# Optimization experiments

Measured on AMD Instinct MI355X. Metric: run time of the kernel, lower is better.

Reference implementation:

```python
import jax, jax.numpy as jnp
import numpy as np

N_NODES = 100000
N_EDGES = 300000
N_GRAPHS = 2048
IN_DIM = 38
HID = 256
LAYERS = 5
OUT_DIM = 1
BN_EPS = 1e-5


def setup_inputs() -> dict:
    key = jax.random.key(0)
    ks = jax.random.split(key, 20)
    x = jax.random.normal(ks[0], (N_NODES, IN_DIM), dtype=jnp.float32)
    edge_index = jax.random.randint(ks[1], (2, N_EDGES), 0, N_NODES, dtype=jnp.int32)
    batch = jnp.sort(jax.random.randint(ks[2], (N_NODES,), 0, N_GRAPHS, dtype=jnp.int32))
    s_in = 1.0 / np.sqrt(IN_DIM)
    s_h = 1.0 / np.sqrt(HID)
    return {
        "x": x,
        "edge_index": edge_index,
        "batch": batch,
        "Wp": jax.random.uniform(ks[3], (IN_DIM, HID), jnp.float32, -s_in, s_in),
        "bp": jnp.zeros((HID,), jnp.float32),
        "eps": jnp.zeros((LAYERS,), jnp.float32),  # train_eps=True, init 0
        "W1s": jax.random.uniform(ks[4], (LAYERS, HID, HID), jnp.float32, -s_h, s_h),
        "b1s": jnp.zeros((LAYERS, HID), jnp.float32),
        "W2s": jax.random.uniform(ks[5], (LAYERS, HID, HID), jnp.float32, -s_h, s_h),
        "b2s": jnp.zeros((LAYERS, HID), jnp.float32),
        "gammas": jnp.ones((LAYERS, HID), jnp.float32),
        "betas": jnp.zeros((LAYERS, HID), jnp.float32),
        "Wr1": jax.random.uniform(ks[6], (HID, HID), jnp.float32, -s_h, s_h),
        "br1": jnp.zeros((HID,), jnp.float32),
        "Wr2": jax.random.uniform(ks[7], (HID, OUT_DIM), jnp.float32, -s_h, s_h),
        "br2": jnp.zeros((OUT_DIM,), jnp.float32),
    }


def _forward(x, edge_index, batch, Wp, bp, eps, W1s, b1s, W2s, b2s,
             gammas, betas, Wr1, br1, Wr2, br2):
    src, dst = edge_index[0], edge_index[1]
    h = x @ Wp + bp  # [N, HID]
    for l in range(LAYERS):
        # GINConv: (1+eps)*h_i + sum_{j->i} h_j  (scatter-add over edges)
        agg = jnp.zeros_like(h).at[dst].add(h[src])
        z = (1.0 + eps[l]) * h + agg
        # 2-layer MLP
        z = jax.nn.relu(z @ W1s[l] + b1s[l]) @ W2s[l] + b2s[l]
        # BatchNorm1d (training-mode batch statistics, biased variance)
        mu = jnp.mean(z, axis=0)
        var = jnp.var(z, axis=0)
        z = (z - mu) * jax.lax.rsqrt(var + BN_EPS) * gammas[l] + betas[l]
        h = jax.nn.relu(z)  # dropout disabled (eval)
    # global mean pool over graphs
    sums = jax.ops.segment_sum(h, batch, num_segments=N_GRAPHS)
    counts = jax.ops.segment_sum(jnp.ones((h.shape[0],), h.dtype), batch,
                                 num_segments=N_GRAPHS)
    pooled = sums / jnp.maximum(counts, 1.0)[:, None]
    # readout MLP (dropout disabled)
    out = jax.nn.relu(pooled @ Wr1 + br1) @ Wr2 + br2
    return out  # [N_GRAPHS, OUT_DIM]


def reference(x, edge_index, batch, Wp, bp, eps, W1s, b1s, W2s, b2s,
              gammas, betas, Wr1, br1, Wr2, br2):
    return _forward(x, edge_index, batch, Wp, bp, eps, W1s, b1s, W2s, b2s,
                    gammas, betas, Wr1, br1, Wr2, br2)
```

## Files before the change

kernel.cpp:

```cpp
#include <hip/hip_runtime.h>

#define N_NODES 100000
#define N_EDGES 300000
#define N_GRAPHS 2048
#define IN_DIM 38
#define HID 256
#define LAYERS 5
#define BN_EPS 1e-5f

#define SCAN_CHUNK 512
#define N_CHUNKS ((N_NODES + SCAN_CHUNK - 1) / SCAN_CHUNK)

#define ROW_PAD 128

typedef unsigned short u16;
typedef unsigned int u32;
typedef __attribute__((ext_vector_type(8))) short short8;
typedef __attribute__((ext_vector_type(4))) unsigned short ushortx4;
typedef __attribute__((ext_vector_type(4))) unsigned int uintx4;
typedef __attribute__((ext_vector_type(4))) float floatx4;

__device__ __forceinline__ unsigned short bf16_rne(float f) {
    unsigned int u = __float_as_uint(f);
    unsigned int r = (u + 0x7fffu + ((u >> 16) & 1u)) >> 16;
    return (unsigned short)r;
}
__device__ __forceinline__ float uf(unsigned short b) {
    return __uint_as_float((unsigned int)b << 16);
}
__device__ __forceinline__ float unpack_pair(u32 w) {
    return uf((unsigned short)(w & 0xffffu)) + uf((unsigned short)(w >> 16));
}
__device__ __forceinline__ void split_bf16(float v, unsigned short& hi,
                                           unsigned short& lo) {
    hi = bf16_rne(v);
    float hf = __uint_as_float((unsigned int)hi << 16);
    lo = (unsigned short)(__float_as_uint(v - hf) >> 16);
}
__device__ __forceinline__ u32 pack_pair(float v) {
    unsigned short hb, lb;
    split_bf16(v, hb, lb);
    return (u32)hb | ((u32)lb << 16);
}
__device__ __forceinline__ void load16_to_lds(const void* g, void* l) {
    __builtin_amdgcn_global_load_lds(
        (const __attribute__((address_space(1))) unsigned int*)g,
        (__attribute__((address_space(3))) unsigned int*)l, 16, 0, 0);
}
__device__ __forceinline__ void bn_params(const float* sums, const float* sumsq,
                                          const float* gammas,
                                          const float* betas, int c, float& sc,
                                          float& sh) {
    const float invN = 1.0f / (float)N_NODES;
    float mu = sums[c] * invN;
    float var = sumsq[c] * invN - mu * mu;
    float rs = rsqrtf(var + BN_EPS);
    float g = gammas[c];
    sc = rs * g;
    sh = betas[c] - mu * rs * g;
}

#define PROJ_CH 64
__global__ __launch_bounds__(256) void proj_kernel(
    const float* __restrict__ x, const float* __restrict__ Wp,
    const float* __restrict__ bp, u32* __restrict__ h) {
    __shared__ float xs[PROJ_CH * IN_DIM];
    int t = threadIdx.x;
    float w[IN_DIM];
#pragma unroll
    for (int k = 0; k < IN_DIM; k++) w[k] = Wp[k * HID + t];
    float b = bp[t];
    int n0 = blockIdx.x * PROJ_CH;
    int count = min(PROJ_CH, N_NODES - n0);
    int total = count * IN_DIM;
    const float* xbase = x + (size_t)n0 * IN_DIM;
    for (int i = t; i < total; i += 256) xs[i] = xbase[i];
    __syncthreads();
    for (int n = 0; n < count; n++) {
        float acc = b;
        const float* xr = &xs[n * IN_DIM];
#pragma unroll
        for (int k = 0; k < IN_DIM; k++) acc = fmaf(xr[k], w[k], acc);
        h[(size_t)(n0 + n) * 256 + t] = pack_pair(acc);
    }
}

__global__ __launch_bounds__(256) void hist_kernel(const int* __restrict__ ei,
                                                   int* __restrict__ deg) {
    int e = blockIdx.x * 256 + threadIdx.x;
    if (e < N_EDGES) atomicAdd(&deg[ei[N_EDGES + e]], 1);
}

__global__ __launch_bounds__(256) void scan1_kernel(const int* __restrict__ deg,
                                                    int* __restrict__ offs,
                                                    int* __restrict__ blocksums) {
    __shared__ int s[SCAN_CHUNK];
    int base = blockIdx.x * SCAN_CHUNK;
    int t = threadIdx.x;
    int i0 = t, i1 = t + 256;
    int g0 = base + i0, g1 = base + i1;
    int o0 = (g0 < N_NODES) ? deg[g0] : 0;
    int o1 = (g1 < N_NODES) ? deg[g1] : 0;
    s[i0] = o0;
    s[i1] = o1;
    __syncthreads();
    for (int off = 1; off < SCAN_CHUNK; off <<= 1) {
        int v0 = (i0 >= off) ? s[i0 - off] : 0;
        int v1 = (i1 >= off) ? s[i1 - off] : 0;
        __syncthreads();
        s[i0] += v0;
        s[i1] += v1;
        __syncthreads();
    }
    if (g0 < N_NODES) offs[g0] = s[i0] - o0;
    if (g1 < N_NODES) offs[g1] = s[i1] - o1;
    if (t == 0) blocksums[blockIdx.x] = s[SCAN_CHUNK - 1];
}

__global__ __launch_bounds__(256) void scan2_kernel(int* __restrict__ blocksums) {
    __shared__ int s[256];
    int t = threadIdx.x;
    int o = (t < N_CHUNKS) ? blocksums[t] : 0;
    s[t] = o;
    __syncthreads();
    for (int off = 1; off < 256; off <<= 1) {
        int v = (t >= off) ? s[t - off] : 0;
        __syncthreads();
        s[t] += v;
        __syncthreads();
    }
    if (t < N_CHUNKS) blocksums[t] = s[t] - o;
}

__global__ __launch_bounds__(256) void scan3_kernel(int* __restrict__ offs,
                                                    const int* __restrict__ blocksums,
                                                    int* __restrict__ cursor) {
    int g = blockIdx.x * 256 + threadIdx.x;
    if (g < N_NODES) {
        int v = offs[g] + blocksums[g / SCAN_CHUNK];
        offs[g] = v;
        cursor[g] = v;
    }
    if (g == 0) offs[N_NODES] = N_EDGES;
}

__global__ __launch_bounds__(256) void fill_kernel(const int* __restrict__ ei,
                                                   int* __restrict__ cursor,
                                                   int* __restrict__ csr_src) {
    int e = blockIdx.x * 256 + threadIdx.x;
    if (e < N_EDGES) {
        int src = ei[e];
        int dst = ei[N_EDGES + e];
        int pos = atomicAdd(&cursor[dst], 1);
        csr_src[pos] = src;
    }
}

__global__ __launch_bounds__(256) void gather_kernel(
    const int* __restrict__ offs, const int* __restrict__ csr_src,
    const u32* __restrict__ zin, u16* __restrict__ zout,
    const float* __restrict__ eps, int layer,
    const float* __restrict__ sums, const float* __restrict__ sumsq,
    const float* __restrict__ gammas, const float* __restrict__ betas,
    int useBN) {
    int wave = threadIdx.x >> 6;
    int lane = threadIdx.x & 63;
    int node = blockIdx.x * 4 + wave;
    if (node >= N_NODES) return;
    float s = 1.0f + eps[layer];
    int c0 = lane * 4;
    int beg = offs[node], end = offs[node + 1];
    uintx4 vself = *(const uintx4*)&zin[(size_t)node * 256 + c0];
    float4 sc = make_float4(1.f, 1.f, 1.f, 1.f);
    float4 sh = make_float4(0.f, 0.f, 0.f, 0.f);
    if (useBN) {
        bn_params(sums, sumsq, gammas, betas, c0 + 0, sc.x, sh.x);
        bn_params(sums, sumsq, gammas, betas, c0 + 1, sc.y, sh.y);
        bn_params(sums, sumsq, gammas, betas, c0 + 2, sc.z, sh.z);
        bn_params(sums, sumsq, gammas, betas, c0 + 3, sc.w, sh.w);
    }
    float acc[4];
    acc[0] = unpack_pair(vself[0]);
    acc[1] = unpack_pair(vself[1]);
    acc[2] = unpack_pair(vself[2]);
    acc[3] = unpack_pair(vself[3]);
    if (useBN) {
        acc[0] = fmaxf(acc[0] * sc.x + sh.x, 0.f);
        acc[1] = fmaxf(acc[1] * sc.y + sh.y, 0.f);
        acc[2] = fmaxf(acc[2] * sc.z + sh.z, 0.f);
        acc[3] = fmaxf(acc[3] * sc.w + sh.w, 0.f);
    }
    acc[0] *= s; acc[1] *= s; acc[2] *= s; acc[3] *= s;

    for (int base = beg; base < end; base += 4) {
        int i0 = csr_src[base];
        int i1 = (base + 1 < end) ? csr_src[base + 1] : i0;
        int i2 = (base + 2 < end) ? csr_src[base + 2] : i0;
        int i3 = (base + 3 < end) ? csr_src[base + 3] : i0;
        uintx4 r0 = *(const uintx4*)&zin[(size_t)i0 * 256 + c0];
        uintx4 r1 = *(const uintx4*)&zin[(size_t)i1 * 256 + c0];
        uintx4 r2 = *(const uintx4*)&zin[(size_t)i2 * 256 + c0];
        uintx4 r3 = *(const uintx4*)&zin[(size_t)i3 * 256 + c0];
#define PROC_ROW(rv)                                                   \
        {                                                              \
            float v0 = unpack_pair(rv[0]);                             \
            float v1 = unpack_pair(rv[1]);                             \
            float v2 = unpack_pair(rv[2]);                             \
            float v3 = unpack_pair(rv[3]);                             \
            if (useBN) {                                               \
                v0 = fmaxf(v0 * sc.x + sh.x, 0.f);                     \
                v1 = fmaxf(v1 * sc.y + sh.y, 0.f);                     \
                v2 = fmaxf(v2 * sc.z + sh.z, 0.f);                     \
                v3 = fmaxf(v3 * sc.w + sh.w, 0.f);                     \
            }                                                          \
            acc[0] += v0; acc[1] += v1; acc[2] += v2; acc[3] += v3;    \
        }
        PROC_ROW(r0);
        if (base + 1 < end) PROC_ROW(r1);
        if (base + 2 < end) PROC_ROW(r2);
        if (base + 3 < end) PROC_ROW(r3);
#undef PROC_ROW
    }
    ushortx4 ho, lo2;
#pragma unroll
    for (int q = 0; q < 4; q++) {
        unsigned short hb, lb;
        split_bf16(acc[q], hb, lb);
        ho[q] = hb;
        lo2[q] = lb;
    }
    *(ushortx4*)&zout[(size_t)node * 512 + c0] = ho;
    *(ushortx4*)&zout[(size_t)node * 512 + 256 + c0] = lo2;
}

__global__ __launch_bounds__(256) void packW_kernel(const float* __restrict__ W1s,
                                                    const float* __restrict__ W2s,
                                                    short8* __restrict__ Wpk8) {
    int id = blockIdx.x * 256 + threadIdx.x;
    int lane = id & 63;
    int fid = (id >> 6) & 127;
    int w = id >> 13;
    int kt = fid >> 4, nt = fid & 15;
    const float* Wsrc = (w < 5) ? W1s + (size_t)w * HID * HID
                                : W2s + (size_t)(w - 5) * HID * HID;
    int k0 = kt * 32 + ((lane >> 4) << 3);
    int n = nt * 16 + (lane & 15);
    short8 hi, lo;
#pragma unroll
    for (int e = 0; e < 8; e++) {
        float v = Wsrc[(size_t)(k0 + e) * HID + n];
        unsigned short hb, lb;
        split_bf16(v, hb, lb);
        hi[e] = (short)hb;
        lo[e] = (short)lb;
    }
    size_t base = (size_t)w * 16384;
    Wpk8[base + (size_t)((0 * 8 + kt) * 16 + nt) * 64 + lane] = hi;
    Wpk8[base + (size_t)((1 * 8 + kt) * 16 + nt) * 64 + lane] = lo;
}

__global__ __launch_bounds__(256, 2) void fused_mlp_kernel(
    const u16* __restrict__ A, const short8* __restrict__ W1m,
    const float* __restrict__ b1, const short8* __restrict__ W2m,
    const float* __restrict__ b2, u32* __restrict__ C, int M,
    float* __restrict__ sums, float* __restrict__ sumsq) {
    __shared__ char lds[65536];
    short8* Zf8 = (short8*)lds;
    u16* Hf = (u16*)lds;
    float* cf = (float*)lds;
    int t = threadIdx.x;
    int lane = t & 63;
    int w = t >> 6;
    int m0 = blockIdx.x * 64;
    int col15 = lane & 15;
    int rgrp = lane >> 4;

    short8 bb[2][8];
    short8 aa[2][8];

#pragma unroll
    for (int q = 0; q < 16; q++) {
        int f = q * 4 + w;
        int p = f >> 5;
        int ki = (f >> 3) & 3;
        int ktl = (f >> 2) & 1;
        int mt = f & 3;
        const u16* src = &A[(size_t)(m0 + mt * 16 + col15) * 512 + p * 256 +
                            ki * 64 + ktl * 32 + (rgrp << 3)];
        load16_to_lds(src, &Zf8[f * 64]);
    }
#pragma unroll
    for (int q = 0; q < 8; q++) {
        int p = q >> 2, j = q & 3;
        bb[0][q] = W1m[((size_t)(p * 8 + 0) * 16 + (w * 4 + j)) * 64 + lane];
    }
    __syncthreads();

    floatx4 acc[4][4];
#pragma unroll
    for (int i = 0; i < 4; i++)
#pragma unroll
        for (int j = 0; j < 4; j++) acc[i][j] = (floatx4)0.0f;

#pragma unroll
    for (int q = 0; q < 8; q++) {
        int p = q >> 2, mt = q & 3;
        aa[0][q] = Zf8[(p * 32 + 0 * 4 + mt) * 64 + lane];
    }

#pragma unroll
    for (int kk = 0; kk < 8; kk++) {
        const int cur = kk & 1, nxt = cur ^ 1;
        if (kk < 7) {
#pragma unroll
            for (int q = 0; q < 8; q++) {
                int p = q >> 2, j = q & 3;
                bb[nxt][q] =
                    W1m[((size_t)(p * 8 + kk + 1) * 16 + (w * 4 + j)) * 64 + lane];
            }
#pragma unroll
            for (int q = 0; q < 8; q++) {
                int p = q >> 2, mt = q & 3;
                aa[nxt][q] = Zf8[(p * 32 + (kk + 1) * 4 + mt) * 64 + lane];
            }
        }
        __builtin_amdgcn_s_setprio(1);
#pragma unroll
        for (int i = 0; i < 4; i++)
#pragma unroll
            for (int j = 0; j < 4; j++) {
                acc[i][j] = __builtin_amdgcn_mfma_f32_16x16x32_bf16(
                    aa[cur][i], bb[cur][j], acc[i][j], 0, 0, 0);
                acc[i][j] = __builtin_amdgcn_mfma_f32_16x16x32_bf16(
                    aa[cur][i], bb[cur][4 + j], acc[i][j], 0, 0, 0);
                acc[i][j] = __builtin_amdgcn_mfma_f32_16x16x32_bf16(
                    aa[cur][4 + i], bb[cur][j], acc[i][j], 0, 0, 0);
            }
        __builtin_amdgcn_s_setprio(0);
    }
    __syncthreads();

#pragma unroll
    for (int q = 0; q < 8; q++) {
        int p = q >> 2, j = q & 3;
        bb[0][q] = W2m[((size_t)(p * 8 + 0) * 16 + (w * 4 + j)) * 64 + lane];
    }
#pragma unroll
    for (int j = 0; j < 4; j++) {
        int col = w * 64 + j * 16 + col15;
        float bv = b1[col];
        int kt2 = col >> 5;
        int colg = (col & 31) >> 3;
        int e = col & 7;
#pragma unroll
        for (int i = 0; i < 4; i++) {
            int lane_a = rgrp * 4 + colg * 16;
#pragma unroll
            for (int r = 0; r < 4; r++) {
                float v = fmaxf(acc[i][j][r] + bv, 0.0f);
                unsigned short hb, lb;
                split_bf16(v, hb, lb);
                Hf[(((0 * 8 + kt2) * 4 + i) * 64 + lane_a + r) * 8 + e] = hb;
                Hf[(((1 * 8 + kt2) * 4 + i) * 64 + lane_a + r) * 8 + e] = lb;
            }
        }
    }
    __syncthreads();

    floatx4 acc2[4][4];
#pragma unroll
    for (int i = 0; i < 4; i++)
#pragma unroll
        for (int j = 0; j < 4; j++) acc2[i][j] = (floatx4)0.0f;

#pragma unroll
    for (int q = 0; q < 8; q++) {
        int p = q >> 2, mt = q & 3;
        aa[0][q] = *(short8*)&Hf[(((p * 8 + 0) * 4 + mt) * 64 + lane) * 8];
    }

#pragma unroll
    for (int kj = 0; kj < 8; kj++) {
        const int cur = kj & 1, nxt = cur ^ 1;
        if (kj < 7) {
#pragma unroll
            for (int q = 0; q < 8; q++) {
                int p = q >> 2, j = q & 3;
                bb[nxt][q] =
                    W2m[((size_t)(p * 8 + kj + 1) * 16 + (w * 4 + j)) * 64 + lane];
            }
#pragma unroll
            for (int q = 0; q < 8; q++) {
                int p = q >> 2, mt = q & 3;
                aa[nxt][q] =
                    *(short8*)&Hf[(((p * 8 + kj + 1) * 4 + mt) * 64 + lane) * 8];
            }
        }
        __builtin_amdgcn_s_setprio(1);
#pragma unroll
        for (int i = 0; i < 4; i++)
#pragma unroll
            for (int j = 0; j < 4; j++) {
                acc2[i][j] = __builtin_amdgcn_mfma_f32_16x16x32_bf16(
                    aa[cur][i], bb[cur][j], acc2[i][j], 0, 0, 0);
                acc2[i][j] = __builtin_amdgcn_mfma_f32_16x16x32_bf16(
                    aa[cur][i], bb[cur][4 + j], acc2[i][j], 0, 0, 0);
                acc2[i][j] = __builtin_amdgcn_mfma_f32_16x16x32_bf16(
                    aa[cur][4 + i], bb[cur][j], acc2[i][j], 0, 0, 0);
            }
        __builtin_amdgcn_s_setprio(0);
    }
    __syncthreads();

#pragma unroll
    for (int j = 0; j < 4; j++) {
        int col = w * 64 + j * 16 + col15;
        float bv = b2[col];
        float csum = 0.f, csq = 0.f;
#pragma unroll
        for (int i = 0; i < 4; i++) {
            int rowb = i * 16 + rgrp * 4;
#pragma unroll
            for (int r = 0; r < 4; r++) {
                float v = acc2[i][j][r] + bv;
                cf[(rowb + r) * 256 + col] = v;
                if (m0 + rowb + r < M) {
                    csum += v;
                    csq += v * v;
                }
            }
        }
        csum += __shfl_xor(csum, 16);
        csum += __shfl_xor(csum, 32);
        csq += __shfl_xor(csq, 16);
        csq += __shfl_xor(csq, 32);
        if (rgrp == 0) {
            atomicAdd(&sums[col], csum);
            atomicAdd(&sumsq[col], csq);
        }
    }
    __syncthreads();
#pragma unroll
    for (int k = 0; k < 16; k++) {
        int fi = (k * 256 + t) * 4;
        int row = fi >> 8, colc = fi & 255;
        int m = m0 + row;
        if (m >= M) continue;
        float4 v4 = *(float4*)&cf[fi];
        uintx4 o;
        o[0] = pack_pair(v4.x);
        o[1] = pack_pair(v4.y);
        o[2] = pack_pair(v4.z);
        o[3] = pack_pair(v4.w);
        *(uintx4*)&C[(size_t)m * 256 + colc] = o;
    }
}

__global__ __launch_bounds__(256) void bounds_kernel(const int* __restrict__ batch,
                                                     int* __restrict__ start) {
    int g = blockIdx.x * 256 + threadIdx.x;
    if (g > N_GRAPHS) return;
    int lo = 0, hi = N_NODES;
    while (lo < hi) {
        int mid = (lo + hi) >> 1;
        if (batch[mid] < g) lo = mid + 1;
        else hi = mid;
    }
    start[g] = lo;
}

__global__ __launch_bounds__(256) void segpool_kernel(
    const u32* __restrict__ z, const int* __restrict__ start,
    const float* __restrict__ sums, const float* __restrict__ sumsq,
    const float* __restrict__ gammas, const float* __restrict__ betas,
    float* __restrict__ pooled) {
    int g = blockIdx.x;
    int c = threadIdx.x;
    float sc, sh;
    bn_params(sums, sumsq, gammas, betas, c, sc, sh);
    int beg = start[g], end = start[g + 1];
    float s = 0.f;
    for (int n = beg; n < end; n++) {
        float v = unpack_pair(z[(size_t)n * 256 + c]);
        s += fmaxf(v * sc + sh, 0.f);
    }
    float inv = 1.0f / fmaxf((float)(end - beg), 1.0f);
    pooled[(size_t)g * HID + c] = s * inv;
}

#define RGK 8
__global__ __launch_bounds__(256) void readout_kernel(
    const float* __restrict__ pooled, const float* __restrict__ Wr1,
    const float* __restrict__ br1, const float* __restrict__ Wr2,
    const float* __restrict__ br2, float* __restrict__ out) {
    __shared__ float p[RGK][HID];
    __shared__ float red[RGK][4];
    int g0 = blockIdx.x * RGK;
    int t = threadIdx.x;
#pragma unroll
    for (int q = 0; q < RGK; q++) p[q][t] = pooled[(size_t)(g0 + q) * HID + t];
    __syncthreads();
    int c = t;
    float acc[RGK];
#pragma unroll
    for (int q = 0; q < RGK; q++) acc[q] = br1[c];
    for (int k = 0; k < HID; k++) {
        float wv = Wr1[k * HID + c];
#pragma unroll
        for (int q = 0; q < RGK; q++) acc[q] = fmaf(p[q][k], wv, acc[q]);
    }
    float w2 = Wr2[c];
#pragma unroll
    for (int q = 0; q < RGK; q++) {
        float v = fmaxf(acc[q], 0.f) * w2;
#pragma unroll
        for (int off = 32; off > 0; off >>= 1) v += __shfl_down(v, off, 64);
        if ((c & 63) == 0) red[q][c >> 6] = v;
    }
    __syncthreads();
    if (t < RGK)
        out[g0 + t] = red[t][0] + red[t][1] + red[t][2] + red[t][3] + br2[0];
}

extern "C" void kernel_launch(void* const* d_in, const int* in_sizes, int n_in,
                              void* d_out, int out_size, void* d_ws, size_t ws_size,
                              hipStream_t stream) {
    const float* x      = (const float*)d_in[0];
    const int*   ei     = (const int*)d_in[1];
    const int*   batch  = (const int*)d_in[2];
    const float* Wp     = (const float*)d_in[3];
    const float* bp     = (const float*)d_in[4];
    const float* eps    = (const float*)d_in[5];
    const float* W1s    = (const float*)d_in[6];
    const float* b1s    = (const float*)d_in[7];
    const float* W2s    = (const float*)d_in[8];
    const float* b2s    = (const float*)d_in[9];
    const float* gammas = (const float*)d_in[10];
    const float* betas  = (const float*)d_in[11];
    const float* Wr1    = (const float*)d_in[12];
    const float* br1    = (const float*)d_in[13];
    const float* Wr2    = (const float*)d_in[14];
    const float* br2    = (const float*)d_in[15];
    float* out = (float*)d_out;

    const size_t ROWS = (size_t)N_NODES + ROW_PAD;
    u32* bufA     = (u32*)d_ws;
    u16* bufB     = (u16*)(bufA + ROWS * 256);
    short8* Wpk8  = (short8*)(bufB + ROWS * 512);
    float* sums   = (float*)(Wpk8 + 10 * 16384);
    float* pooled = sums + LAYERS * 512;
    int* start     = (int*)(pooled + (size_t)N_GRAPHS * HID);
    int* deg       = start + N_GRAPHS + 1;
    int* offs      = deg + N_NODES;
    int* cursor    = offs + N_NODES + 1;
    int* csr_src   = cursor + N_NODES;
    int* blocksums = csr_src + N_EDGES;

    hipMemsetAsync(deg, 0, N_NODES * sizeof(int), stream);
    hipMemsetAsync(sums, 0, LAYERS * 512 * sizeof(float), stream);
    hist_kernel<<<(N_EDGES + 255) / 256, 256, 0, stream>>>(ei, deg);
    scan1_kernel<<<N_CHUNKS, 256, 0, stream>>>(deg, offs, blocksums);
    scan2_kernel<<<1, 256, 0, stream>>>(blocksums);
    scan3_kernel<<<(N_NODES + 255) / 256, 256, 0, stream>>>(offs, blocksums,
                                                            cursor);
    fill_kernel<<<(N_EDGES + 255) / 256, 256, 0, stream>>>(ei, cursor, csr_src);
    packW_kernel<<<320, 256, 0, stream>>>(W1s, W2s, Wpk8);
    bounds_kernel<<<(N_GRAPHS + 1 + 255) / 256, 256, 0, stream>>>(batch, start);

    proj_kernel<<<(N_NODES + PROJ_CH - 1) / PROJ_CH, 256, 0, stream>>>(x, Wp, bp,
                                                                       bufA);

    const int MLP_BLOCKS = (N_NODES + 63) / 64;
    for (int l = 0; l < LAYERS; l++) {
        float* lsums = sums + l * 512;
        float* lsumsq = lsums + 256;
        const float* psums = sums + (l - 1) * 512;
        gather_kernel<<<(N_NODES + 3) / 4, 256, 0, stream>>>(
            offs, csr_src, bufA, bufB, eps, l,
            l > 0 ? psums : sums, l > 0 ? psums + 256 : sums,
            gammas + (l > 0 ? (l - 1) : 0) * HID,
            betas + (l > 0 ? (l - 1) : 0) * HID, l > 0 ? 1 : 0);
        fused_mlp_kernel<<<MLP_BLOCKS, 256, 0, stream>>>(
            bufB, Wpk8 + (size_t)l * 16384, b1s + l * HID,
            Wpk8 + (size_t)(5 + l) * 16384, b2s + l * HID, bufA, N_NODES,
            lsums, lsumsq);
    }

    segpool_kernel<<<N_GRAPHS, 256, 0, stream>>>(
        bufA, start, sums + 4 * 512, sums + 4 * 512 + 256, gammas + 4 * HID,
        betas + 4 * HID, pooled);
    readout_kernel<<<N_GRAPHS / RGK, 256, 0, stream>>>(pooled, Wr1, br1, Wr2, br2,
                                                       out);
}
```

Baseline: 1.062 ms.

## Fuse neighbor gather into MLP kernel, writing aggregated rows straight to swizzled LDS

The separate gather kernel is removed. Each MLP block now aggregates its own 64 nodes (self term, optional BN+ReLU, neighbor sum) and writes the hi/lo bf16 split directly into LDS with an XOR swizzle, instead of round-tripping through a global buffer loaded with global_load_lds. Activations now ping-pong between two u32 buffers, since the gathered input can no longer be overwritten in place. This removes the intermediate global write/read and a launch per layer, but the latency-bound gather now runs inside an occupancy-limited MFMA kernel (launch bounds 256,2) with no overlap against the matmul.

Measured after the change: 1.124 ms. +5.8%, slower.

```diff
diff --git a/kernel.cpp b/kernel.cpp
--- a/kernel.cpp
+++ b/kernel.cpp
@@ -42,10 +42,8 @@
     split_bf16(v, hb, lb);
     return (u32)hb | ((u32)lb << 16);
 }
-__device__ __forceinline__ void load16_to_lds(const void* g, void* l) {
-    __builtin_amdgcn_global_load_lds(
-        (const __attribute__((address_space(1))) unsigned int*)g,
-        (__attribute__((address_space(3))) unsigned int*)l, 16, 0, 0);
+__device__ __forceinline__ int swz(int b) {
+    return b ^ (((b >> 8) & 3) << 4) ^ (((b >> 12) & 1) << 6);
 }
 __device__ __forceinline__ void bn_params(const float* sums, const float* sumsq,
                                           const float* gammas,
@@ -154,83 +152,6 @@
         int pos = atomicAdd(&cursor[dst], 1);
         csr_src[pos] = src;
     }
-}
-
-__global__ __launch_bounds__(256) void gather_kernel(
-    const int* __restrict__ offs, const int* __restrict__ csr_src,
-    const u32* __restrict__ zin, u16* __restrict__ zout,
-    const float* __restrict__ eps, int layer,
-    const float* __restrict__ sums, const float* __restrict__ sumsq,
-    const float* __restrict__ gammas, const float* __restrict__ betas,
-    int useBN) {
-    int wave = threadIdx.x >> 6;
-    int lane = threadIdx.x & 63;
-    int node = blockIdx.x * 4 + wave;
-    if (node >= N_NODES) return;
-    float s = 1.0f + eps[layer];
-    int c0 = lane * 4;
-    int beg = offs[node], end = offs[node + 1];
-    uintx4 vself = *(const uintx4*)&zin[(size_t)node * 256 + c0];
-    float4 sc = make_float4(1.f, 1.f, 1.f, 1.f);
-    float4 sh = make_float4(0.f, 0.f, 0.f, 0.f);
-    if (useBN) {
-        bn_params(sums, sumsq, gammas, betas, c0 + 0, sc.x, sh.x);
-        bn_params(sums, sumsq, gammas, betas, c0 + 1, sc.y, sh.y);
-        bn_params(sums, sumsq, gammas, betas, c0 + 2, sc.z, sh.z);
-        bn_params(sums, sumsq, gammas, betas, c0 + 3, sc.w, sh.w);
-    }
-    float acc[4];
-    acc[0] = unpack_pair(vself[0]);
-    acc[1] = unpack_pair(vself[1]);
-    acc[2] = unpack_pair(vself[2]);
-    acc[3] = unpack_pair(vself[3]);
-    if (useBN) {
-        acc[0] = fmaxf(acc[0] * sc.x + sh.x, 0.f);
-        acc[1] = fmaxf(acc[1] * sc.y + sh.y, 0.f);
-        acc[2] = fmaxf(acc[2] * sc.z + sh.z, 0.f);
-        acc[3] = fmaxf(acc[3] * sc.w + sh.w, 0.f);
-    }
-    acc[0] *= s; acc[1] *= s; acc[2] *= s; acc[3] *= s;
-
-    for (int base = beg; base < end; base += 4) {
-        int i0 = csr_src[base];
-        int i1 = (base + 1 < end) ? csr_src[base + 1] : i0;
-        int i2 = (base + 2 < end) ? csr_src[base + 2] : i0;
-        int i3 = (base + 3 < end) ? csr_src[base + 3] : i0;
-        uintx4 r0 = *(const uintx4*)&zin[(size_t)i0 * 256 + c0];
-        uintx4 r1 = *(const uintx4*)&zin[(size_t)i1 * 256 + c0];
-        uintx4 r2 = *(const uintx4*)&zin[(size_t)i2 * 256 + c0];
-        uintx4 r3 = *(const uintx4*)&zin[(size_t)i3 * 256 + c0];
-#define PROC_ROW(rv)                                                   \
-        {                                                              \
-            float v0 = unpack_pair(rv[0]);                             \
-            float v1 = unpack_pair(rv[1]);                             \
-            float v2 = unpack_pair(rv[2]);                             \
-            float v3 = unpack_pair(rv[3]);                             \
-            if (useBN) {                                               \
-                v0 = fmaxf(v0 * sc.x + sh.x, 0.f);                     \
-                v1 = fmaxf(v1 * sc.y + sh.y, 0.f);                     \
-                v2 = fmaxf(v2 * sc.z + sh.z, 0.f);                     \
-                v3 = fmaxf(v3 * sc.w + sh.w, 0.f);                     \
-            }                                                          \
-            acc[0] += v0; acc[1] += v1; acc[2] += v2; acc[3] += v3;    \
-        }
-        PROC_ROW(r0);
-        if (base + 1 < end) PROC_ROW(r1);
-        if (base + 2 < end) PROC_ROW(r2);
-        if (base + 3 < end) PROC_ROW(r3);
-#undef PROC_ROW
-    }
-    ushortx4 ho, lo2;
-#pragma unroll
-    for (int q = 0; q < 4; q++) {
-        unsigned short hb, lb;
-        split_bf16(acc[q], hb, lb);
-        ho[q] = hb;
-        lo2[q] = lb;
-    }
-    *(ushortx4*)&zout[(size_t)node * 512 + c0] = ho;
-    *(ushortx4*)&zout[(size_t)node * 512 + 256 + c0] = lo2;
 }
 
 __global__ __launch_bounds__(256) void packW_kernel(const float* __restrict__ W1s,
@@ -260,12 +181,15 @@
 }
 
 __global__ __launch_bounds__(256, 2) void fused_mlp_kernel(
-    const u16* __restrict__ A, const short8* __restrict__ W1m,
-    const float* __restrict__ b1, const short8* __restrict__ W2m,
-    const float* __restrict__ b2, u32* __restrict__ C, int M,
-    float* __restrict__ sums, float* __restrict__ sumsq) {
+    const u32* __restrict__ zin, const int* __restrict__ offs,
+    const int* __restrict__ csr_src, const float* __restrict__ eps, int layer,
+    const float* __restrict__ psums, const float* __restrict__ psumsq,
+    const float* __restrict__ pgam, const float* __restrict__ pbet, int useBN,
+    const short8* __restrict__ W1m, const float* __restrict__ b1,
+    const short8* __restrict__ W2m, const float* __restrict__ b2,
+    u32* __restrict__ C, int M, float* __restrict__ sums,
+    float* __restrict__ sumsq) {
     __shared__ char lds[65536];
-    short8* Zf8 = (short8*)lds;
     u16* Hf = (u16*)lds;
     float* cf = (float*)lds;
     int t = threadIdx.x;
@@ -278,16 +202,79 @@
     short8 bb[2][8];
     short8 aa[2][8];
 
-#pragma unroll
-    for (int q = 0; q < 16; q++) {
-        int f = q * 4 + w;
-        int p = f >> 5;
-        int ki = (f >> 3) & 3;
-        int ktl = (f >> 2) & 1;
-        int mt = f & 3;
-        const u16* src = &A[(size_t)(m0 + mt * 16 + col15) * 512 + p * 256 +
-                            ki * 64 + ktl * 32 + (rgrp << 3)];
-        load16_to_lds(src, &Zf8[f * 64]);
+    {
+        float s = 1.0f + eps[layer];
+        int c0 = lane * 4;
+        float4 sc = make_float4(1.f, 1.f, 1.f, 1.f);
+        float4 sh = make_float4(0.f, 0.f, 0.f, 0.f);
+        if (useBN) {
+            bn_params(psums, psumsq, pgam, pbet, c0 + 0, sc.x, sh.x);
+            bn_params(psums, psumsq, pgam, pbet, c0 + 1, sc.y, sh.y);
+            bn_params(psums, psumsq, pgam, pbet, c0 + 2, sc.z, sh.z);
+            bn_params(psums, psumsq, pgam, pbet, c0 + 3, sc.w, sh.w);
+        }
+        int fb0 = ((lane >> 4) * 8 + ((lane >> 3) & 1) * 4 + w) * 1024 +
+                  ((lane >> 1) & 3) * 256 + (lane & 1) * 8;
+        for (int g = 0; g < 16; g++) {
+            int node = m0 + w * 16 + g;
+            float acc[4] = {0.f, 0.f, 0.f, 0.f};
+            if (node < N_NODES) {
+                int beg = offs[node], end = offs[node + 1];
+                uintx4 vs = *(const uintx4*)&zin[(size_t)node * 256 + c0];
+                acc[0] = unpack_pair(vs[0]);
+                acc[1] = unpack_pair(vs[1]);
+                acc[2] = unpack_pair(vs[2]);
+                acc[3] = unpack_pair(vs[3]);
+                if (useBN) {
+                    acc[0] = fmaxf(acc[0] * sc.x + sh.x, 0.f);
+                    acc[1] = fmaxf(acc[1] * sc.y + sh.y, 0.f);
+                    acc[2] = fmaxf(acc[2] * sc.z + sh.z, 0.f);
+                    acc[3] = fmaxf(acc[3] * sc.w + sh.w, 0.f);
+                }
+                acc[0] *= s; acc[1] *= s; acc[2] *= s; acc[3] *= s;
+                for (int base = beg; base < end; base += 4) {
+                    int i0 = csr_src[base];
+                    int i1 = (base + 1 < end) ? csr_src[base + 1] : i0;
+                    int i2 = (base + 2 < end) ? csr_src[base + 2] : i0;
+                    int i3 = (base + 3 < end) ? csr_src[base + 3] : i0;
+                    uintx4 r0 = *(const uintx4*)&zin[(size_t)i0 * 256 + c0];
+                    uintx4 r1 = *(const uintx4*)&zin[(size_t)i1 * 256 + c0];
+                    uintx4 r2 = *(const uintx4*)&zin[(size_t)i2 * 256 + c0];
+                    uintx4 r3 = *(const uintx4*)&zin[(size_t)i3 * 256 + c0];
+#define PROC_ROW(rv)                                                   \
+                    {                                                  \
+                        float v0 = unpack_pair(rv[0]);                 \
+                        float v1 = unpack_pair(rv[1]);                 \
+                        float v2 = unpack_pair(rv[2]);                 \
+                        float v3 = unpack_pair(rv[3]);                 \
+                        if (useBN) {                                   \
+                            v0 = fmaxf(v0 * sc.x + sh.x, 0.f);         \
+                            v1 = fmaxf(v1 * sc.y + sh.y, 0.f);         \
+                            v2 = fmaxf(v2 * sc.z + sh.z, 0.f);         \
+                            v3 = fmaxf(v3 * sc.w + sh.w, 0.f);         \
+                        }                                              \
+                        acc[0] += v0; acc[1] += v1;                    \
+                        acc[2] += v2; acc[3] += v3;                    \
+                    }
+                    PROC_ROW(r0);
+                    if (base + 1 < end) PROC_ROW(r1);
+                    if (base + 2 < end) PROC_ROW(r2);
+                    if (base + 3 < end) PROC_ROW(r3);
+#undef PROC_ROW
+                }
+            }
+            ushortx4 ho, lo2;
+#pragma unroll
+            for (int q = 0; q < 4; q++) {
+                unsigned short hb, lb;
+                split_bf16(acc[q], hb, lb);
+                ho[q] = hb;
+                lo2[q] = lb;
+            }
+            int sb = swz(fb0 + g * 16);
+            *(ushortx4*)(lds + sb) = ho;
+            *(ushortx4*)(lds + sb + 32768) = lo2;
+        }
     }
 #pragma unroll
     for (int q = 0; q < 8; q++) {
@@ -305,7 +292,7 @@
 #pragma unroll
     for (int q = 0; q < 8; q++) {
         int p = q >> 2, mt = q & 3;
-        aa[0][q] = Zf8[(p * 32 + 0 * 4 + mt) * 64 + lane];
+        aa[0][q] = *(short8*)(lds + swz(((p * 32 + mt) * 64 + lane) * 16));
     }
 
 #pragma unroll
@@ -321,7 +308,8 @@
 #pragma unroll
             for (int q = 0; q < 8; q++) {
                 int p = q >> 2, mt = q & 3;
-                aa[nxt][q] = Zf8[(p * 32 + (kk + 1) * 4 + mt) * 64 + lane];
+                aa[nxt][q] = *(short8*)(
+                    lds + swz(((p * 32 + (kk + 1) * 4 + mt) * 64 + lane) * 16));
             }
         }
         __builtin_amdgcn_s_setprio(1);
@@ -545,8 +533,8 @@
 
     const size_t ROWS = (size_t)N_NODES + ROW_PAD;
     u32* bufA     = (u32*)d_ws;
-    u16* bufB     = (u16*)(bufA + ROWS * 256);
-    short8* Wpk8  = (short8*)(bufB + ROWS * 512);
+    u32* bufC     = bufA + ROWS * 256;
+    short8* Wpk8  = (short8*)(bufC + ROWS * 256);
     float* sums   = (float*)(Wpk8 + 10 * 16384);
     float* pooled = sums + LAYERS * 512;
     int* start     = (int*)(pooled + (size_t)N_GRAPHS * HID);
@@ -571,23 +559,25 @@
                                                                        bufA);
 
     const int MLP_BLOCKS = (N_NODES + 63) / 64;
+    u32* zin = bufA;
+    u32* zout = bufC;
     for (int l = 0; l < LAYERS; l++) {
         float* lsums = sums + l * 512;
         float* lsumsq = lsums + 256;
         const float* psums = sums + (l - 1) * 512;
-        gather_kernel<<<(N_NODES + 3) / 4, 256, 0, stream>>>(
-            offs, csr_src, bufA, bufB, eps, l,
+        fused_mlp_kernel<<<MLP_BLOCKS, 256, 0, stream>>>(
+            zin, offs, csr_src, eps, l,
             l > 0 ? psums : sums, l > 0 ? psums + 256 : sums,
             gammas + (l > 0 ? (l - 1) : 0) * HID,
-            betas + (l > 0 ? (l - 1) : 0) * HID, l > 0 ? 1 : 0);
-        fused_mlp_kernel<<<MLP_BLOCKS, 256, 0, stream>>>(
-            bufB, Wpk8 + (size_t)l * 16384, b1s + l * HID,
-            Wpk8 + (size_t)(5 + l) * 16384, b2s + l * HID, bufA, N_NODES,
+            betas + (l > 0 ? (l - 1) : 0) * HID, l > 0 ? 1 : 0,
+            Wpk8 + (size_t)l * 16384, b1s + l * HID,
+            Wpk8 + (size_t)(5 + l) * 16384, b2s + l * HID, zout, N_NODES,
             lsums, lsumsq);
+        u32* tmp = zin; zin = zout; zout = tmp;
     }
 
     segpool_kernel<<<N_GRAPHS, 256, 0, stream>>>(
-        bufA, start, sums + 4 * 512, sums + 4 * 512 + 256, gammas + 4 * HID,
+        zin, start, sums + 4 * 512, sums + 4 * 512 + 256, gammas + 4 * HID,
         betas + 4 * HID, pooled);
     readout_kernel<<<N_GRAPHS / RGK, 256, 0, stream>>>(pooled, Wr1, br1, Wr2, br2,
                                                        out);
```
